# Performance work log

Hardware: AMD Instinct MI355X
Metric: run time of the kernel (lower is better)

Reference implementation:

```python
import jax, jax.numpy as jnp
import numpy as np

N = 50000      # nodes
E = 1600000    # edges (avg degree 32)
F_IN = 3       # PROTEINS num_node_features
H = 64         # dim_h
G = 512        # num graphs in batch
C = 2          # PROTEINS num_classes
BN_EPS = 1e-5


def setup_inputs() -> dict:
    key = jax.random.key(0)
    ks = iter(jax.random.split(key, 64))

    def rn(shape, s=0.1):
        return (jax.random.normal(next(ks), shape) * s).astype(jnp.float32)

    inp = {"x": rn((N, F_IN), 1.0)}
    for li, din in ((1, F_IN), (2, H), (3, H)):
        p = f"conv{li}_"
        inp[p + "w1"] = rn((din, H))
        inp[p + "b1"] = rn((H,))
        inp[p + "bn_g"] = jnp.ones((H,), jnp.float32)
        inp[p + "bn_b"] = jnp.zeros((H,), jnp.float32)
        inp[p + "bn_m"] = rn((H,))
        inp[p + "bn_v"] = jax.random.uniform(next(ks), (H,), jnp.float32, 0.5, 1.5)
        inp[p + "w2"] = rn((H, H))
        inp[p + "b2"] = rn((H,))
    inp["lin1_w"] = rn((3 * H, 3 * H))
    inp["lin1_b"] = rn((3 * H,))
    inp["lin2_w"] = rn((3 * H, C))
    inp["lin2_b"] = rn((C,))
    inp["edge_index"] = jax.random.randint(next(ks), (2, E), 0, N, jnp.int64)
    inp["batch"] = jnp.sort(jax.random.randint(next(ks), (N,), 0, G, jnp.int64))
    return inp


def gin_conv(x, src, dst, w1, b1, g, bb, m, v, w2, b2):
    # GINConv, eps=0: mlp(x + sum_{j->i} x_j); aggregate messages at target (dst)
    agg = jax.ops.segment_sum(x[src], dst, num_segments=N)  # [N, d]
    h = x + agg
    h = h @ w1 + b1
    h = (h - m) * jax.lax.rsqrt(v + BN_EPS) * g + bb  # BatchNorm1d (eval)
    h = jax.nn.relu(h)
    h = jax.nn.relu(h @ w2 + b2)
    return h


def reference(x,
              conv1_w1, conv1_b1, conv1_bn_g, conv1_bn_b, conv1_bn_m, conv1_bn_v, conv1_w2, conv1_b2,
              conv2_w1, conv2_b1, conv2_bn_g, conv2_bn_b, conv2_bn_m, conv2_bn_v, conv2_w2, conv2_b2,
              conv3_w1, conv3_b1, conv3_bn_g, conv3_bn_b, conv3_bn_m, conv3_bn_v, conv3_w2, conv3_b2,
              lin1_w, lin1_b, lin2_w, lin2_b,
              edge_index, batch):
    src, dst = edge_index[0], edge_index[1]
    h1 = gin_conv(x,  src, dst, conv1_w1, conv1_b1, conv1_bn_g, conv1_bn_b, conv1_bn_m, conv1_bn_v, conv1_w2, conv1_b2)
    h2 = gin_conv(h1, src, dst, conv2_w1, conv2_b1, conv2_bn_g, conv2_bn_b, conv2_bn_m, conv2_bn_v, conv2_w2, conv2_b2)
    h3 = gin_conv(h2, src, dst, conv3_w1, conv3_b1, conv3_bn_g, conv3_bn_b, conv3_bn_m, conv3_bn_v, conv3_w2, conv3_b2)
    # global_add_pool per graph
    p1 = jax.ops.segment_sum(h1, batch, num_segments=G)
    p2 = jax.ops.segment_sum(h2, batch, num_segments=G)
    p3 = jax.ops.segment_sum(h3, batch, num_segments=G)
    h = jnp.concatenate((p1, p2, p3), axis=1)          # [G, 3H]
    h = jax.nn.relu(h @ lin1_w + lin1_b)
    # dropout p=0.5 is identity in eval mode
    h = h @ lin2_w + lin2_b                            # [G, C]
    return (h, jax.nn.log_softmax(h, axis=1))
```

## Files before the change

### kernel.cpp

```cpp
#include <hip/hip_runtime.h>
#include <hip/hip_bf16.h>
#include <math.h>

#define N_NODES 50000
#define N_EDGES 1600000
#define H 64
#define G_GRAPHS 512
#define C_CLS 2
#define BN_EPS 1e-5f
#define NBUCK 196
#define BUCKCAP 16384
#define E4 (N_EDGES / 4)
#define CSR_BLOCKS ((E4 + 511) / 512)
#define IOP 72

typedef __attribute__((ext_vector_type(8))) short short8;
typedef __attribute__((ext_vector_type(4))) float floatx4;

__device__ __forceinline__ float bflo(unsigned int u) { return __uint_as_float(u << 16); }
__device__ __forceinline__ float bfhi(unsigned int u) { return __uint_as_float(u & 0xffff0000u); }
__device__ __forceinline__ unsigned int bf16_rne(float f) {
    unsigned int u = __float_as_uint(f);
    u += 0x7fffu + ((u >> 16) & 1u);
    return u >> 16;
}

__global__ __launch_bounds__(256) void prep_kernel(
    const float* __restrict__ w2_0, const float* __restrict__ w1_1,
    const float* __restrict__ w2_1, const float* __restrict__ w1_2,
    const float* __restrict__ w2_2, unsigned short* __restrict__ wt,
    const float* __restrict__ x, uint2* __restrict__ xb) {
    int b = blockIdx.x, t = threadIdx.x;
    if (b < 5) {
        const float* w = (b == 0) ? w2_0 : (b == 1) ? w1_1 : (b == 2) ? w2_1
                         : (b == 3) ? w1_2 : w2_2;
        unsigned short* o = wt + b * (H * H);
        for (int idx = t; idx < H * H; idx += 256) {
            int k = idx >> 6, j = idx & 63;
            o[j * H + k] = (unsigned short)bf16_rne(w[idx]);
        }
    } else {
        int node = (b - 5) * 256 + t;
        if (node < N_NODES) {
            uint2 p;
            p.x = bf16_rne(x[node * 3 + 0]) | (bf16_rne(x[node * 3 + 1]) << 16);
            p.y = bf16_rne(x[node * 3 + 2]);
            xb[node] = p;
        }
    }
}

__global__ __launch_bounds__(256) void scatter1_kernel(const int* __restrict__ src,
                                                       const int* __restrict__ dst,
                                                       int* __restrict__ gcnt,
                                                       int* __restrict__ gpacked) {
    __shared__ int bh[NBUCK];
    int t = threadIdx.x;
    if (t < NBUCK) bh[t] = 0;
    __syncthreads();
    int base = blockIdx.x * 512;

    int pkA[4], bkA[4], lrA[4]; bool vA = false;
    int pkB[4], bkB[4], lrB[4]; bool vB = false;
    {
        int i = base + t;
        if (i < E4) {
            vA = true;
            int4 s4 = ((const int4*)src)[i];
            int4 d4 = ((const int4*)dst)[i];
            bkA[0] = d4.x >> 8; pkA[0] = ((d4.x & 255) << 16) | s4.x; lrA[0] = atomicAdd(&bh[bkA[0]], 1);
            bkA[1] = d4.y >> 8; pkA[1] = ((d4.y & 255) << 16) | s4.y; lrA[1] = atomicAdd(&bh[bkA[1]], 1);
            bkA[2] = d4.z >> 8; pkA[2] = ((d4.z & 255) << 16) | s4.z; lrA[2] = atomicAdd(&bh[bkA[2]], 1);
            bkA[3] = d4.w >> 8; pkA[3] = ((d4.w & 255) << 16) | s4.w; lrA[3] = atomicAdd(&bh[bkA[3]], 1);
        }
    }
    {
        int i = base + 256 + t;
        if (i < E4) {
            vB = true;
            int4 s4 = ((const int4*)src)[i];
            int4 d4 = ((const int4*)dst)[i];
            bkB[0] = d4.x >> 8; pkB[0] = ((d4.x & 255) << 16) | s4.x; lrB[0] = atomicAdd(&bh[bkB[0]], 1);
            bkB[1] = d4.y >> 8; pkB[1] = ((d4.y & 255) << 16) | s4.y; lrB[1] = atomicAdd(&bh[bkB[1]], 1);
            bkB[2] = d4.z >> 8; pkB[2] = ((d4.z & 255) << 16) | s4.z; lrB[2] = atomicAdd(&bh[bkB[2]], 1);
            bkB[3] = d4.w >> 8; pkB[3] = ((d4.w & 255) << 16) | s4.w; lrB[3] = atomicAdd(&bh[bkB[3]], 1);
        }
    }
    __syncthreads();
    if (t < NBUCK) {
        int c = bh[t];
        bh[t] = c ? atomicAdd(&gcnt[t], c) : 0;
    }
    __syncthreads();
    if (vA) {
#pragma unroll
        for (int q = 0; q < 4; q++) gpacked[bkA[q] * BUCKCAP + bh[bkA[q]] + lrA[q]] = pkA[q];
    }
    if (vB) {
#pragma unroll
        for (int q = 0; q < 4; q++) gpacked[bkB[q] * BUCKCAP + bh[bkB[q]] + lrB[q]] = pkB[q];
    }
}

__global__ __launch_bounds__(256) void bcsr_kernel(const int* __restrict__ gpacked,
                                                   const int* __restrict__ gcnt,
                                                   int* __restrict__ row_start,
                                                   int* __restrict__ edge_src) {
    __shared__ int cnt[256];
    __shared__ int pref[256];
    int b = blockIdx.x;
    int t = threadIdx.x;

    int v = (t < NBUCK) ? gcnt[t] : 0;
    pref[t] = v;
    __syncthreads();
    for (int off = 1; off < 256; off <<= 1) {
        int u = 0;
        if (t >= off) u = pref[t - off];
        __syncthreads();
        if (t >= off) pref[t] += u;
        __syncthreads();
    }
    int bs = (b > 0) ? pref[b - 1] : 0;
    int cnt_b = gcnt[b];
    if (b == 0 && t == 0) row_start[N_NODES] = N_EDGES;
    __syncthreads();

    const int* gp = gpacked + (size_t)b * BUCKCAP;
    cnt[t] = 0;
    __syncthreads();
    for (int i = t; i < cnt_b; i += 256) atomicAdd(&cnt[gp[i] >> 16], 1);
    __syncthreads();
    int c = cnt[t];
    pref[t] = c;
    __syncthreads();
    for (int off = 1; off < 256; off <<= 1) {
        int u = 0;
        if (t >= off) u = pref[t - off];
        __syncthreads();
        if (t >= off) pref[t] += u;
        __syncthreads();
    }
    int excl = pref[t] - c;
    int node = b * 256 + t;
    if (node < N_NODES) row_start[node] = bs + excl;
    cnt[t] = excl;
    __syncthreads();
    for (int i = t; i < cnt_b; i += 256) {
        int p = gp[i];
        int pos = atomicAdd(&cnt[p >> 16], 1);
        edge_src[bs + pos] = p & 0xffff;
    }
}

#define RED3(A) { A += __shfl_xor(A, 8); A += __shfl_xor(A, 16); A += __shfl_xor(A, 32); }
#define RED6(A) { A += __shfl_xor(A, 1); A += __shfl_xor(A, 2); A += __shfl_xor(A, 4); \
                  A += __shfl_xor(A, 8); A += __shfl_xor(A, 16); A += __shfl_xor(A, 32); }

__global__ __launch_bounds__(512) void gin1_fused16_kernel(
    const float* __restrict__ x, const uint2* __restrict__ xb,
    const int* __restrict__ row_start, const int* __restrict__ edge_src,
    const float* __restrict__ w1, const float* __restrict__ b1,
    const float* __restrict__ bn_g, const float* __restrict__ bn_b,
    const float* __restrict__ bn_m, const float* __restrict__ bn_v,
    const unsigned short* __restrict__ w2t, const float* __restrict__ b2,
    __hip_bfloat16* __restrict__ hout, const int* __restrict__ batch,
    float* __restrict__ pool) {
    __shared__ unsigned short s_mid[16 * IOP];
    __shared__ int s_bat[16];

    int tid = threadIdx.x;
    int wave = tid >> 6, j = tid & 63;
    int nodebase = blockIdx.x * 16;
    if (tid < 16) s_bat[tid] = batch[nodebase + tid];

    float wj0 = w1[j], wj1 = w1[H + j], wj2 = w1[2 * H + j];
    float sc = rsqrtf(bn_v[j] + BN_EPS) * bn_g[j];
    float sh = bn_b[j] - bn_m[j] * sc;
    float bj = b1[j];

    int n0 = nodebase + wave * 2;
    int rs0 = row_start[n0];
    int re0 = row_start[n0 + 1];
    int re1 = row_start[n0 + 2];
    int c0 = re0 - rs0;
    int total = re1 - rs0;

    float a00 = 0.f, a01 = 0.f, a02 = 0.f;
    float a10 = 0.f, a11 = 0.f, a12 = 0.f;
    for (int base = 0; base < total; base += 64) {
        int idx = rs0 + base + j;
        if (idx < re1) {
            uint2 p = xb[edge_src[idx]];
            if (base + j < c0) { a00 += bflo(p.x); a01 += bfhi(p.x); a02 += bflo(p.y); }
            else               { a10 += bflo(p.x); a11 += bfhi(p.x); a12 += bflo(p.y); }
        }
    }
    RED6(a00) RED6(a01) RED6(a02)
    RED6(a10) RED6(a11) RED6(a12)
    {
        float in0 = a00 + x[n0 * 3 + 0];
        float in1 = a01 + x[n0 * 3 + 1];
        float in2 = a02 + x[n0 * 3 + 2];
        float m = bj + in0 * wj0 + in1 * wj1 + in2 * wj2;
        m = fmaxf(m * sc + sh, 0.f);
        s_mid[(wave * 2) * IOP + j] = (unsigned short)bf16_rne(m);
    }
    {
        int n1 = n0 + 1;
        float in0 = a10 + x[n1 * 3 + 0];
        float in1 = a11 + x[n1 * 3 + 1];
        float in2 = a12 + x[n1 * 3 + 2];
        float m = bj + in0 * wj0 + in1 * wj1 + in2 * wj2;
        m = fmaxf(m * sc + sh, 0.f);
        s_mid[(wave * 2 + 1) * IOP + j] = (unsigned short)bf16_rne(m);
    }
    __syncthreads();

    if (wave == 0) {
        int quad = j >> 4, l15 = j & 15;
        float bb2[4];
#pragma unroll
        for (int jt = 0; jt < 4; jt++) bb2[jt] = b2[jt * 16 + l15];

        short8 m0 = *(const short8*)&s_mid[l15 * IOP + quad * 8];
        short8 m1 = *(const short8*)&s_mid[l15 * IOP + quad * 8 + 32];
        int bq0 = s_bat[quad * 4], bq3 = s_bat[quad * 4 + 3];
#pragma unroll
        for (int jt = 0; jt < 4; jt++) {
            short8 b0 = *(const short8*)&w2t[(jt * 16 + l15) * H + quad * 8];
            short8 bv = *(const short8*)&w2t[(jt * 16 + l15) * H + quad * 8 + 32];
            floatx4 c = {0.f, 0.f, 0.f, 0.f};
            c = __builtin_amdgcn_mfma_f32_16x16x32_bf16(m0, b0, c, 0, 0, 0);
            c = __builtin_amdgcn_mfma_f32_16x16x32_bf16(m1, bv, c, 0, 0, 0);
            float vv[4];
#pragma unroll
            for (int r = 0; r < 4; r++) {
                float v = fmaxf(c[r] + bb2[jt], 0.f);
                vv[r] = v;
                s_mid[(quad * 4 + r) * IOP + jt * 16 + l15] = (unsigned short)bf16_rne(v);
            }
            int jj = jt * 16 + l15;
            if (bq0 == bq3) {
                atomicAdd(&pool[bq0 * 192 + jj], (vv[0] + vv[1]) + (vv[2] + vv[3]));
            } else {
                atomicAdd(&pool[s_bat[quad * 4 + 0] * 192 + jj], vv[0]);
                atomicAdd(&pool[s_bat[quad * 4 + 1] * 192 + jj], vv[1]);
                atomicAdd(&pool[s_bat[quad * 4 + 2] * 192 + jj], vv[2]);
                atomicAdd(&pool[s_bat[quad * 4 + 3] * 192 + jj], vv[3]);
            }
        }
        unsigned short* ho = (unsigned short*)hout;
#pragma unroll
        for (int cc = 0; cc < 2; cc++) {
            int r = cc * 8 + (j >> 3);
            short8 v = *(const short8*)&s_mid[r * IOP + (j & 7) * 8];
            *(short8*)(ho + (size_t)(nodebase + r) * H + (j & 7) * 8) = v;
        }
    }
}

#define ACC8(R, A0, A1, A2, A3, A4, A5, A6, A7) { \
    A0 += bflo(R.x); A1 += bfhi(R.x); A2 += bflo(R.y); A3 += bfhi(R.y); \
    A4 += bflo(R.z); A5 += bfhi(R.z); A6 += bflo(R.w); A7 += bfhi(R.w); }

#define GROUP_ACC(R, r) { \
    if ((r) < lim) { \
        if ((base + (r)) < c0) { ACC8(R, a00, a01, a02, a03, a04, a05, a06, a07) } \
        else                   { ACC8(R, a10, a11, a12, a13, a14, a15, a16, a17) } \
    } }

__global__ __launch_bounds__(512) void gin_fused16_kernel(
    const __hip_bfloat16* __restrict__ hin, const int* __restrict__ row_start,
    const int* __restrict__ edge_src,
    const unsigned short* __restrict__ w1t, const float* __restrict__ b1,
    const float* __restrict__ bn_g, const float* __restrict__ bn_b,
    const float* __restrict__ bn_m, const float* __restrict__ bn_v,
    const unsigned short* __restrict__ w2t, const float* __restrict__ b2,
    __hip_bfloat16* __restrict__ hout, const int* __restrict__ batch,
    float* __restrict__ pool) {
    __shared__ unsigned short s_xs[16 * IOP];
    __shared__ unsigned short s_mid[16 * IOP];
    __shared__ int s_bat[16];

    int tid = threadIdx.x;
    int wave = tid >> 6, j = tid & 63;
    int o = j >> 3, jo = j & 7;
    int nodebase = blockIdx.x * 16;
    if (tid < 16) s_bat[tid] = batch[nodebase + tid];

    const char* hb = (const char*)hin;

    int n0 = nodebase + wave * 2;
    int rs0 = row_start[n0];
    int re0 = row_start[n0 + 1];
    int re1 = row_start[n0 + 2];
    int c0 = re0 - rs0;
    int total = re1 - rs0;

    float a00 = 0.f, a01 = 0.f, a02 = 0.f, a03 = 0.f, a04 = 0.f, a05 = 0.f, a06 = 0.f, a07 = 0.f;
    float a10 = 0.f, a11 = 0.f, a12 = 0.f, a13 = 0.f, a14 = 0.f, a15 = 0.f, a16 = 0.f, a17 = 0.f;

    for (int base = 0; base < total; base += 64) {
        int idx = rs0 + base + j;
        int sv = (idx < re1) ? edge_src[idx] : 0;
        int lim = min(64, total - base);
#pragma unroll
        for (int i = 0; i < 64; i += 32) {
            if (i >= lim) break;
            int r0 = i + o, r1 = i + 8 + o, r2 = i + 16 + o, r3 = i + 24 + o;
            int s0 = __shfl(sv, r0);
            int s1 = __shfl(sv, r1);
            int s2 = __shfl(sv, r2);
            int s3 = __shfl(sv, r3);
            uint4 R0 = *(const uint4*)(hb + (size_t)s0 * 128 + jo * 16);
            uint4 R1 = *(const uint4*)(hb + (size_t)s1 * 128 + jo * 16);
            uint4 R2 = *(const uint4*)(hb + (size_t)s2 * 128 + jo * 16);
            uint4 R3 = *(const uint4*)(hb + (size_t)s3 * 128 + jo * 16);
            GROUP_ACC(R0, r0)
            GROUP_ACC(R1, r1)
            GROUP_ACC(R2, r2)
            GROUP_ACC(R3, r3)
        }
    }
    RED3(a00) RED3(a01) RED3(a02) RED3(a03) RED3(a04) RED3(a05) RED3(a06) RED3(a07)
    RED3(a10) RED3(a11) RED3(a12) RED3(a13) RED3(a14) RED3(a15) RED3(a16) RED3(a17)

    if (o < 2) {
        int nl = wave * 2 + o;
        float r0 = (o == 0) ? a00 : a10, r1 = (o == 0) ? a01 : a11;
        float r2 = (o == 0) ? a02 : a12, r3 = (o == 0) ? a03 : a13;
        float r4 = (o == 0) ? a04 : a14, r5 = (o == 0) ? a05 : a15;
        float r6 = (o == 0) ? a06 : a16, r7 = (o == 0) ? a07 : a17;
        uint4 raw = *(const uint4*)(hb + (size_t)(nodebase + nl) * 128 + jo * 16);
        r0 += bflo(raw.x); r1 += bfhi(raw.x);
        r2 += bflo(raw.y); r3 += bfhi(raw.y);
        r4 += bflo(raw.z); r5 += bfhi(raw.z);
        r6 += bflo(raw.w); r7 += bfhi(raw.w);
        uint4 ov;
        ov.x = bf16_rne(r0) | (bf16_rne(r1) << 16);
        ov.y = bf16_rne(r2) | (bf16_rne(r3) << 16);
        ov.z = bf16_rne(r4) | (bf16_rne(r5) << 16);
        ov.w = bf16_rne(r6) | (bf16_rne(r7) << 16);
        *(uint4*)&s_xs[nl * IOP + jo * 8] = ov;
    }
    __syncthreads();

    if (wave == 0) {
        int quad = j >> 4, l15 = j & 15;
        float scl[4], sht[4], bb1[4], bb2[4];
#pragma unroll
        for (int jt = 0; jt < 4; jt++) {
            int jj = jt * 16 + l15;
            float sc = rsqrtf(bn_v[jj] + BN_EPS) * bn_g[jj];
            scl[jt] = sc;
            sht[jt] = bn_b[jj] - bn_m[jj] * sc;
            bb1[jt] = b1[jj];
            bb2[jt] = b2[jj];
        }
        short8 a0 = *(const short8*)&s_xs[l15 * IOP + quad * 8];
        short8 a1 = *(const short8*)&s_xs[l15 * IOP + quad * 8 + 32];
#pragma unroll
        for (int jt = 0; jt < 4; jt++) {
            short8 b0 = *(const short8*)&w1t[(jt * 16 + l15) * H + quad * 8];
            short8 bv = *(const short8*)&w1t[(jt * 16 + l15) * H + quad * 8 + 32];
            floatx4 c = {0.f, 0.f, 0.f, 0.f};
            c = __builtin_amdgcn_mfma_f32_16x16x32_bf16(a0, b0, c, 0, 0, 0);
            c = __builtin_amdgcn_mfma_f32_16x16x32_bf16(a1, bv, c, 0, 0, 0);
#pragma unroll
            for (int r = 0; r < 4; r++) {
                float v = (c[r] + bb1[jt]) * scl[jt] + sht[jt];
                v = fmaxf(v, 0.f);
                s_mid[(quad * 4 + r) * IOP + jt * 16 + l15] = (unsigned short)bf16_rne(v);
            }
        }
        short8 m0 = *(const short8*)&s_mid[l15 * IOP + quad * 8];
        short8 m1 = *(const short8*)&s_mid[l15 * IOP + quad * 8 + 32];
        int bq0 = s_bat[quad * 4], bq3 = s_bat[quad * 4 + 3];
#pragma unroll
        for (int jt = 0; jt < 4; jt++) {
            short8 b0 = *(const short8*)&w2t[(jt * 16 + l15) * H + quad * 8];
            short8 bv = *(const short8*)&w2t[(jt * 16 + l15) * H + quad * 8 + 32];
            floatx4 c = {0.f, 0.f, 0.f, 0.f};
            c = __builtin_amdgcn_mfma_f32_16x16x32_bf16(m0, b0, c, 0, 0, 0);
            c = __builtin_amdgcn_mfma_f32_16x16x32_bf16(m1, bv, c, 0, 0, 0);
            float vv[4];
#pragma unroll
            for (int r = 0; r < 4; r++) {
                float v = fmaxf(c[r] + bb2[jt], 0.f);
                vv[r] = v;
                s_xs[(quad * 4 + r) * IOP + jt * 16 + l15] = (unsigned short)bf16_rne(v);
            }
            int jj = jt * 16 + l15;
            if (bq0 == bq3) {
                atomicAdd(&pool[bq0 * 192 + jj], (vv[0] + vv[1]) + (vv[2] + vv[3]));
            } else {
                atomicAdd(&pool[s_bat[quad * 4 + 0] * 192 + jj], vv[0]);
                atomicAdd(&pool[s_bat[quad * 4 + 1] * 192 + jj], vv[1]);
                atomicAdd(&pool[s_bat[quad * 4 + 2] * 192 + jj], vv[2]);
                atomicAdd(&pool[s_bat[quad * 4 + 3] * 192 + jj], vv[3]);
            }
        }
        unsigned short* ho = (unsigned short*)hout;
#pragma unroll
        for (int cc = 0; cc < 2; cc++) {
            int r = cc * 8 + (j >> 3);
            short8 v = *(const short8*)&s_xs[r * IOP + (j & 7) * 8];
            *(short8*)(ho + (size_t)(nodebase + r) * H + (j & 7) * 8) = v;
        }
    }
}

__global__ __launch_bounds__(192) void head_kernel(
    const float* __restrict__ pool,
    const float* __restrict__ lin1_w, const float* __restrict__ lin1_b,
    const float* __restrict__ lin2_w, const float* __restrict__ lin2_b,
    float* __restrict__ out) {
    __shared__ float s_row[3 * H];
    __shared__ float s_mid[3 * H];
    __shared__ float s_z[C_CLS];

    int g = blockIdx.x;
    int j = threadIdx.x;
    s_row[j] = pool[g * 192 + j];
    __syncthreads();

    float acc = lin1_b[j];
    for (int k = 0; k < 3 * H; k++) acc += s_row[k] * lin1_w[k * (3 * H) + j];
    s_mid[j] = fmaxf(acc, 0.f);
    __syncthreads();

    if (j < C_CLS) {
        float z = lin2_b[j];
        for (int k = 0; k < 3 * H; k++) z += s_mid[k] * lin2_w[k * C_CLS + j];
        s_z[j] = z;
    }
    __syncthreads();
    if (j < C_CLS) {
        float z0 = s_z[0], z1 = s_z[1];
        float mx = fmaxf(z0, z1);
        float lse = mx + logf(expf(z0 - mx) + expf(z1 - mx));
        out[g * C_CLS + j] = s_z[j];
        out[G_GRAPHS * C_CLS + g * C_CLS + j] = s_z[j] - lse;
    }
}

extern "C" void kernel_launch(void* const* d_in, const int* in_sizes, int n_in,
                              void* d_out, int out_size, void* d_ws, size_t ws_size,
                              hipStream_t stream) {
    const float* x = (const float*)d_in[0];
    const float* cw1[3], *cb1[3], *cg[3], *cbb[3], *cm[3], *cv[3], *cw2[3], *cb2[3];
    for (int l = 0; l < 3; l++) {
        int b = 1 + 8 * l;
        cw1[l] = (const float*)d_in[b + 0];
        cb1[l] = (const float*)d_in[b + 1];
        cg[l]  = (const float*)d_in[b + 2];
        cbb[l] = (const float*)d_in[b + 3];
        cm[l]  = (const float*)d_in[b + 4];
        cv[l]  = (const float*)d_in[b + 5];
        cw2[l] = (const float*)d_in[b + 6];
        cb2[l] = (const float*)d_in[b + 7];
    }
    const float* lin1_w = (const float*)d_in[25];
    const float* lin1_b = (const float*)d_in[26];
    const float* lin2_w = (const float*)d_in[27];
    const float* lin2_b = (const float*)d_in[28];
    const int* edge_index = (const int*)d_in[29];
    const int* batch = (const int*)d_in[30];
    const int* src = edge_index;
    const int* dst = edge_index + N_EDGES;
    float* out = (float*)d_out;

    int* edge_src = (int*)d_ws;
    int* gpacked = edge_src + N_EDGES;
    int* gcnt = gpacked + (size_t)NBUCK * BUCKCAP;
    float* pool = (float*)(gcnt + NBUCK);
    int* row_start = (int*)(pool + G_GRAPHS * 3 * H);
    uintptr_t hp = (uintptr_t)(row_start + N_NODES + 2);
    hp = (hp + 127) & ~(uintptr_t)127;
    unsigned short* wt = (unsigned short*)hp;
    uint2* xb = (uint2*)(wt + 5 * H * H);
    __hip_bfloat16* h1 = (__hip_bfloat16*)(xb + N_NODES);
    __hip_bfloat16* h2 = h1 + (size_t)N_NODES * H;
    __hip_bfloat16* h3 = h2 + (size_t)N_NODES * H;

    const unsigned short* w2t_0 = wt + 0 * H * H;
    const unsigned short* w1t_1 = wt + 1 * H * H;
    const unsigned short* w2t_1 = wt + 2 * H * H;
    const unsigned short* w1t_2 = wt + 3 * H * H;
    const unsigned short* w2t_2 = wt + 4 * H * H;

    hipMemsetAsync(gcnt, 0, NBUCK * sizeof(int) + G_GRAPHS * 3 * H * sizeof(float), stream);
    prep_kernel<<<5 + (N_NODES + 255) / 256, 256, 0, stream>>>(
        cw2[0], cw1[1], cw2[1], cw1[2], cw2[2], wt, x, xb);
    scatter1_kernel<<<CSR_BLOCKS, 256, 0, stream>>>(src, dst, gcnt, gpacked);
    bcsr_kernel<<<NBUCK, 256, 0, stream>>>(gpacked, gcnt, row_start, edge_src);

    const int fgrid = N_NODES / 16;

    gin1_fused16_kernel<<<fgrid, 512, 0, stream>>>(x, xb, row_start, edge_src,
        cw1[0], cb1[0], cg[0], cbb[0], cm[0], cv[0], w2t_0, cb2[0], h1, batch, pool);
    gin_fused16_kernel<<<fgrid, 512, 0, stream>>>(h1, row_start, edge_src,
        w1t_1, cb1[1], cg[1], cbb[1], cm[1], cv[1], w2t_1, cb2[1], h2, batch, pool + 64);
    gin_fused16_kernel<<<fgrid, 512, 0, stream>>>(h2, row_start, edge_src,
        w1t_2, cb1[2], cg[2], cbb[2], cm[2], cv[2], w2t_2, cb2[2], h3, batch, pool + 128);
    head_kernel<<<G_GRAPHS, 3 * H, 0, stream>>>(pool,
        lin1_w, lin1_b, lin2_w, lin2_b, out);
}
```

Measured before the change: 289.4 us.

## Merge prep and scatter kernels, split MFMA across waves, decouple per-node gathers

The weight/x prep kernel and the edge bucket-scatter kernel become one launch, which also zeroes a padding row in h1/h2. The layer-1 gather now loops per node, and in the hidden layers each wave gathers its two nodes independently, with out-of-range lanes pointed at the zero row instead of branching per edge. The MLP matmuls are spread across four waves (one 16-column tile each) rather than done by a single wave, and launch bounds of 4 blocks per CU are added. The aim is less launch overhead, more parallel MFMA work in the epilogue and less divergence in the gather, at the cost of extra block barriers and a __syncthreads that only waves 0-3 reach inside the wave<4 branch (waves 4-7 call one in the else branch).

```diff
diff --git a/kernel.cpp b/kernel.cpp
--- a/kernel.cpp
+++ b/kernel.cpp
@@ -11,8 +11,11 @@
 #define NBUCK 196
 #define BUCKCAP 16384
 #define E4 (N_EDGES / 4)
-#define CSR_BLOCKS ((E4 + 511) / 512)
+#define SCHUNKS ((E4 + 511) / 512)
+#define XCHUNKS ((N_NODES + 255) / 256)
 #define IOP 72
+#define ZROW N_NODES
+#define HSTRIDE ((N_NODES + 1) * H)
 
 typedef __attribute__((ext_vector_type(8))) short short8;
 typedef __attribute__((ext_vector_type(4))) float floatx4;
@@ -25,80 +28,85 @@
     return u >> 16;
 }
 
-__global__ __launch_bounds__(256) void prep_kernel(
+#define RED3(A) { A += __shfl_xor(A, 8); A += __shfl_xor(A, 16); A += __shfl_xor(A, 32); }
+#define RED6(A) { A += __shfl_xor(A, 1); A += __shfl_xor(A, 2); A += __shfl_xor(A, 4); \
+                  A += __shfl_xor(A, 8); A += __shfl_xor(A, 16); A += __shfl_xor(A, 32); }
+
+__global__ __launch_bounds__(256) void prepscatter_kernel(
+    const int* __restrict__ src, const int* __restrict__ dst,
+    int* __restrict__ gcnt, int* __restrict__ gpacked,
     const float* __restrict__ w2_0, const float* __restrict__ w1_1,
     const float* __restrict__ w2_1, const float* __restrict__ w1_2,
     const float* __restrict__ w2_2, unsigned short* __restrict__ wt,
-    const float* __restrict__ x, uint2* __restrict__ xb) {
+    const float* __restrict__ x, uint2* __restrict__ xb,
+    __hip_bfloat16* __restrict__ h1, __hip_bfloat16* __restrict__ h2) {
     int b = blockIdx.x, t = threadIdx.x;
-    if (b < 5) {
-        const float* w = (b == 0) ? w2_0 : (b == 1) ? w1_1 : (b == 2) ? w2_1
-                         : (b == 3) ? w1_2 : w2_2;
-        unsigned short* o = wt + b * (H * H);
+    if (b < SCHUNKS) {
+        __shared__ int bh[NBUCK];
+        if (t < NBUCK) bh[t] = 0;
+        __syncthreads();
+        int base = b * 512;
+        int pkA[4], bkA[4], lrA[4]; bool vA = false;
+        int pkB[4], bkB[4], lrB[4]; bool vB = false;
+        {
+            int i = base + t;
+            if (i < E4) {
+                vA = true;
+                int4 s4 = ((const int4*)src)[i];
+                int4 d4 = ((const int4*)dst)[i];
+                bkA[0] = d4.x >> 8; pkA[0] = ((d4.x & 255) << 16) | s4.x; lrA[0] = atomicAdd(&bh[bkA[0]], 1);
+                bkA[1] = d4.y >> 8; pkA[1] = ((d4.y & 255) << 16) | s4.y; lrA[1] = atomicAdd(&bh[bkA[1]], 1);
+                bkA[2] = d4.z >> 8; pkA[2] = ((d4.z & 255) << 16) | s4.z; lrA[2] = atomicAdd(&bh[bkA[2]], 1);
+                bkA[3] = d4.w >> 8; pkA[3] = ((d4.w & 255) << 16) | s4.w; lrA[3] = atomicAdd(&bh[bkA[3]], 1);
+            }
+        }
+        {
+            int i = base + 256 + t;
+            if (i < E4) {
+                vB = true;
+                int4 s4 = ((const int4*)src)[i];
+                int4 d4 = ((const int4*)dst)[i];
+                bkB[0] = d4.x >> 8; pkB[0] = ((d4.x & 255) << 16) | s4.x; lrB[0] = atomicAdd(&bh[bkB[0]], 1);
+                bkB[1] = d4.y >> 8; pkB[1] = ((d4.y & 255) << 16) | s4.y; lrB[1] = atomicAdd(&bh[bkB[1]], 1);
+                bkB[2] = d4.z >> 8; pkB[2] = ((d4.z & 255) << 16) | s4.z; lrB[2] = atomicAdd(&bh[bkB[2]], 1);
+                bkB[3] = d4.w >> 8; pkB[3] = ((d4.w & 255) << 16) | s4.w; lrB[3] = atomicAdd(&bh[bkB[3]], 1);
+            }
+        }
+        __syncthreads();
+        if (t < NBUCK) {
+            int c = bh[t];
+            bh[t] = c ? atomicAdd(&gcnt[t], c) : 0;
+        }
+        __syncthreads();
+        if (vA) {
+#pragma unroll
+            for (int q = 0; q < 4; q++) gpacked[bkA[q] * BUCKCAP + bh[bkA[q]] + lrA[q]] = pkA[q];
+        }
+        if (vB) {
+#pragma unroll
+            for (int q = 0; q < 4; q++) gpacked[bkB[q] * BUCKCAP + bh[bkB[q]] + lrB[q]] = pkB[q];
+        }
+    } else if (b < SCHUNKS + 5) {
+        int w_id = b - SCHUNKS;
+        const float* w = (w_id == 0) ? w2_0 : (w_id == 1) ? w1_1 : (w_id == 2) ? w2_1
+                         : (w_id == 3) ? w1_2 : w2_2;
+        unsigned short* o = wt + w_id * (H * H);
         for (int idx = t; idx < H * H; idx += 256) {
-            int k = idx >> 6, j = idx & 63;
-            o[j * H + k] = (unsigned short)bf16_rne(w[idx]);
-        }
-    } else {
-        int node = (b - 5) * 256 + t;
+            int k = idx >> 6, jc = idx & 63;
+            o[jc * H + k] = (unsigned short)bf16_rne(w[idx]);
+        }
+    } else if (b < SCHUNKS + 5 + XCHUNKS) {
+        int node = (b - SCHUNKS - 5) * 256 + t;
         if (node < N_NODES) {
             uint2 p;
             p.x = bf16_rne(x[node * 3 + 0]) | (bf16_rne(x[node * 3 + 1]) << 16);
             p.y = bf16_rne(x[node * 3 + 2]);
             xb[node] = p;
         }
-    }
-}
-
-__global__ __launch_bounds__(256) void scatter1_kernel(const int* __restrict__ src,
-                                                       const int* __restrict__ dst,
-                                                       int* __restrict__ gcnt,
-                                                       int* __restrict__ gpacked) {
-    __shared__ int bh[NBUCK];
-    int t = threadIdx.x;
-    if (t < NBUCK) bh[t] = 0;
-    __syncthreads();
-    int base = blockIdx.x * 512;
-
-    int pkA[4], bkA[4], lrA[4]; bool vA = false;
-    int pkB[4], bkB[4], lrB[4]; bool vB = false;
-    {
-        int i = base + t;
-        if (i < E4) {
-            vA = true;
-            int4 s4 = ((const int4*)src)[i];
-            int4 d4 = ((const int4*)dst)[i];
-            bkA[0] = d4.x >> 8; pkA[0] = ((d4.x & 255) << 16) | s4.x; lrA[0] = atomicAdd(&bh[bkA[0]], 1);
-            bkA[1] = d4.y >> 8; pkA[1] = ((d4.y & 255) << 16) | s4.y; lrA[1] = atomicAdd(&bh[bkA[1]], 1);
-            bkA[2] = d4.z >> 8; pkA[2] = ((d4.z & 255) << 16) | s4.z; lrA[2] = atomicAdd(&bh[bkA[2]], 1);
-            bkA[3] = d4.w >> 8; pkA[3] = ((d4.w & 255) << 16) | s4.w; lrA[3] = atomicAdd(&bh[bkA[3]], 1);
-        }
-    }
-    {
-        int i = base + 256 + t;
-        if (i < E4) {
-            vB = true;
-            int4 s4 = ((const int4*)src)[i];
-            int4 d4 = ((const int4*)dst)[i];
-            bkB[0] = d4.x >> 8; pkB[0] = ((d4.x & 255) << 16) | s4.x; lrB[0] = atomicAdd(&bh[bkB[0]], 1);
-            bkB[1] = d4.y >> 8; pkB[1] = ((d4.y & 255) << 16) | s4.y; lrB[1] = atomicAdd(&bh[bkB[1]], 1);
-            bkB[2] = d4.z >> 8; pkB[2] = ((d4.z & 255) << 16) | s4.z; lrB[2] = atomicAdd(&bh[bkB[2]], 1);
-            bkB[3] = d4.w >> 8; pkB[3] = ((d4.w & 255) << 16) | s4.w; lrB[3] = atomicAdd(&bh[bkB[3]], 1);
-        }
-    }
-    __syncthreads();
-    if (t < NBUCK) {
-        int c = bh[t];
-        bh[t] = c ? atomicAdd(&gcnt[t], c) : 0;
-    }
-    __syncthreads();
-    if (vA) {
-#pragma unroll
-        for (int q = 0; q < 4; q++) gpacked[bkA[q] * BUCKCAP + bh[bkA[q]] + lrA[q]] = pkA[q];
-    }
-    if (vB) {
-#pragma unroll
-        for (int q = 0; q < 4; q++) gpacked[bkB[q] * BUCKCAP + bh[bkB[q]] + lrB[q]] = pkB[q];
+    } else {
+        uint4 z = {0u, 0u, 0u, 0u};
+        if (t < 8) ((uint4*)((unsigned short*)h1 + (size_t)ZROW * H))[t] = z;
+        else if (t < 16) ((uint4*)((unsigned short*)h2 + (size_t)ZROW * H))[t - 8] = z;
     }
 }
 
@@ -152,10 +160,6 @@
         edge_src[bs + pos] = p & 0xffff;
     }
 }
-
-#define RED3(A) { A += __shfl_xor(A, 8); A += __shfl_xor(A, 16); A += __shfl_xor(A, 32); }
-#define RED6(A) { A += __shfl_xor(A, 1); A += __shfl_xor(A, 2); A += __shfl_xor(A, 4); \
-                  A += __shfl_xor(A, 8); A += __shfl_xor(A, 16); A += __shfl_xor(A, 32); }
 
 __global__ __launch_bounds__(512) void gin1_fused16_kernel(
     const float* __restrict__ x, const uint2* __restrict__ xb,
@@ -167,10 +171,12 @@
     __hip_bfloat16* __restrict__ hout, const int* __restrict__ batch,
     float* __restrict__ pool) {
     __shared__ unsigned short s_mid[16 * IOP];
+    __shared__ unsigned short s_xs[16 * IOP];
     __shared__ int s_bat[16];
 
     int tid = threadIdx.x;
     int wave = tid >> 6, j = tid & 63;
+    int quad = j >> 4, l15 = j & 15;
     int nodebase = blockIdx.x * 16;
     if (tid < 16) s_bat[tid] = batch[nodebase + tid];
 
@@ -179,98 +185,67 @@
     float sh = bn_b[j] - bn_m[j] * sc;
     float bj = b1[j];
 
-    int n0 = nodebase + wave * 2;
-    int rs0 = row_start[n0];
-    int re0 = row_start[n0 + 1];
-    int re1 = row_start[n0 + 2];
-    int c0 = re0 - rs0;
-    int total = re1 - rs0;
-
-    float a00 = 0.f, a01 = 0.f, a02 = 0.f;
-    float a10 = 0.f, a11 = 0.f, a12 = 0.f;
-    for (int base = 0; base < total; base += 64) {
-        int idx = rs0 + base + j;
-        if (idx < re1) {
-            uint2 p = xb[edge_src[idx]];
-            if (base + j < c0) { a00 += bflo(p.x); a01 += bfhi(p.x); a02 += bflo(p.y); }
-            else               { a10 += bflo(p.x); a11 += bfhi(p.x); a12 += bflo(p.y); }
-        }
-    }
-    RED6(a00) RED6(a01) RED6(a02)
-    RED6(a10) RED6(a11) RED6(a12)
-    {
-        float in0 = a00 + x[n0 * 3 + 0];
-        float in1 = a01 + x[n0 * 3 + 1];
-        float in2 = a02 + x[n0 * 3 + 2];
+    for (int nl = wave * 2; nl < wave * 2 + 2; nl++) {
+        int node = nodebase + nl;
+        int rs = row_start[node], re = row_start[node + 1];
+        float a0 = 0.f, a1 = 0.f, a2 = 0.f;
+        for (int t2 = rs + j; t2 < re; t2 += 64) {
+            uint2 p = xb[edge_src[t2]];
+            a0 += bflo(p.x); a1 += bfhi(p.x); a2 += bflo(p.y);
+        }
+        RED6(a0) RED6(a1) RED6(a2)
+        float in0 = a0 + x[node * 3 + 0];
+        float in1 = a1 + x[node * 3 + 1];
+        float in2 = a2 + x[node * 3 + 2];
         float m = bj + in0 * wj0 + in1 * wj1 + in2 * wj2;
         m = fmaxf(m * sc + sh, 0.f);
-        s_mid[(wave * 2) * IOP + j] = (unsigned short)bf16_rne(m);
-    }
-    {
-        int n1 = n0 + 1;
-        float in0 = a10 + x[n1 * 3 + 0];
-        float in1 = a11 + x[n1 * 3 + 1];
-        float in2 = a12 + x[n1 * 3 + 2];
-        float m = bj + in0 * wj0 + in1 * wj1 + in2 * wj2;
-        m = fmaxf(m * sc + sh, 0.f);
-        s_mid[(wave * 2 + 1) * IOP + j] = (unsigned short)bf16_rne(m);
-    }
-    __syncthreads();
-
-    if (wave == 0) {
-        int quad = j >> 4, l15 = j & 15;
-        float bb2[4];
-#pragma unroll
-        for (int jt = 0; jt < 4; jt++) bb2[jt] = b2[jt * 16 + l15];
-
+        s_mid[nl * IOP + j] = (unsigned short)bf16_rne(m);
+    }
+    __syncthreads();
+
+    if (wave < 4) {
+        int jj = wave * 16 + l15;
+        float bb2 = b2[jj];
         short8 m0 = *(const short8*)&s_mid[l15 * IOP + quad * 8];
         short8 m1 = *(const short8*)&s_mid[l15 * IOP + quad * 8 + 32];
+        short8 b0 = *(const short8*)&w2t[jj * H + quad * 8];
+        short8 bv = *(const short8*)&w2t[jj * H + quad * 8 + 32];
+        floatx4 c = {0.f, 0.f, 0.f, 0.f};
+        c = __builtin_amdgcn_mfma_f32_16x16x32_bf16(m0, b0, c, 0, 0, 0);
+        c = __builtin_amdgcn_mfma_f32_16x16x32_bf16(m1, bv, c, 0, 0, 0);
+        float vv[4];
+#pragma unroll
+        for (int r = 0; r < 4; r++) {
+            vv[r] = fmaxf(c[r] + bb2, 0.f);
+            s_xs[(quad * 4 + r) * IOP + jj] = (unsigned short)bf16_rne(vv[r]);
+        }
         int bq0 = s_bat[quad * 4], bq3 = s_bat[quad * 4 + 3];
-#pragma unroll
-        for (int jt = 0; jt < 4; jt++) {
-            short8 b0 = *(const short8*)&w2t[(jt * 16 + l15) * H + quad * 8];
-            short8 bv = *(const short8*)&w2t[(jt * 16 + l15) * H + quad * 8 + 32];
-            floatx4 c = {0.f, 0.f, 0.f, 0.f};
-            c = __builtin_amdgcn_mfma_f32_16x16x32_bf16(m0, b0, c, 0, 0, 0);
-            c = __builtin_amdgcn_mfma_f32_16x16x32_bf16(m1, bv, c, 0, 0, 0);
-            float vv[4];
-#pragma unroll
-            for (int r = 0; r < 4; r++) {
-                float v = fmaxf(c[r] + bb2[jt], 0.f);
-                vv[r] = v;
-                s_mid[(quad * 4 + r) * IOP + jt * 16 + l15] = (unsigned short)bf16_rne(v);
-            }
-            int jj = jt * 16 + l15;
-            if (bq0 == bq3) {
-                atomicAdd(&pool[bq0 * 192 + jj], (vv[0] + vv[1]) + (vv[2] + vv[3]));
-            } else {
-                atomicAdd(&pool[s_bat[quad * 4 + 0] * 192 + jj], vv[0]);
-                atomicAdd(&pool[s_bat[quad * 4 + 1] * 192 + jj], vv[1]);
-                atomicAdd(&pool[s_bat[quad * 4 + 2] * 192 + jj], vv[2]);
-                atomicAdd(&pool[s_bat[quad * 4 + 3] * 192 + jj], vv[3]);
-            }
-        }
-        unsigned short* ho = (unsigned short*)hout;
-#pragma unroll
-        for (int cc = 0; cc < 2; cc++) {
-            int r = cc * 8 + (j >> 3);
-            short8 v = *(const short8*)&s_mid[r * IOP + (j & 7) * 8];
-            *(short8*)(ho + (size_t)(nodebase + r) * H + (j & 7) * 8) = v;
-        }
-    }
-}
-
-#define ACC8(R, A0, A1, A2, A3, A4, A5, A6, A7) { \
-    A0 += bflo(R.x); A1 += bfhi(R.x); A2 += bflo(R.y); A3 += bfhi(R.y); \
-    A4 += bflo(R.z); A5 += bfhi(R.z); A6 += bflo(R.w); A7 += bfhi(R.w); }
-
-#define GROUP_ACC(R, r) { \
-    if ((r) < lim) { \
-        if ((base + (r)) < c0) { ACC8(R, a00, a01, a02, a03, a04, a05, a06, a07) } \
-        else                   { ACC8(R, a10, a11, a12, a13, a14, a15, a16, a17) } \
-    } }
-
-__global__ __launch_bounds__(512) void gin_fused16_kernel(
+        if (bq0 == bq3) {
+            atomicAdd(&pool[bq0 * 192 + jj], (vv[0] + vv[1]) + (vv[2] + vv[3]));
+        } else {
+            atomicAdd(&pool[s_bat[quad * 4 + 0] * 192 + jj], vv[0]);
+            atomicAdd(&pool[s_bat[quad * 4 + 1] * 192 + jj], vv[1]);
+            atomicAdd(&pool[s_bat[quad * 4 + 2] * 192 + jj], vv[2]);
+            atomicAdd(&pool[s_bat[quad * 4 + 3] * 192 + jj], vv[3]);
+        }
+    }
+    __syncthreads();
+
+    if (wave < 2) {
+        int r = wave * 8 + (j >> 3);
+        short8 v = *(const short8*)&s_xs[r * IOP + (j & 7) * 8];
+        *(short8*)((unsigned short*)hout + (size_t)(nodebase + r) * H + (j & 7) * 8) = v;
+    }
+}
+
+#define ACCA(R) { \
+    a0 += bflo(R.x); a1 += bfhi(R.x); a2 += bflo(R.y); a3 += bfhi(R.y); \
+    a4 += bflo(R.z); a5 += bfhi(R.z); a6 += bflo(R.w); a7 += bfhi(R.w); }
+#define ACCB(R) { \
+    b0 += bflo(R.x); b1 += bfhi(R.x); b2 += bflo(R.y); b3 += bfhi(R.y); \
+    b4 += bflo(R.z); b5 += bfhi(R.z); b6 += bflo(R.w); b7 += bfhi(R.w); }
+
+__global__ __launch_bounds__(512, 4) void gin_fused16_kernel(
     const __hip_bfloat16* __restrict__ hin, const int* __restrict__ row_start,
     const int* __restrict__ edge_src,
     const unsigned short* __restrict__ w1t, const float* __restrict__ b1,
@@ -286,52 +261,66 @@
     int tid = threadIdx.x;
     int wave = tid >> 6, j = tid & 63;
     int o = j >> 3, jo = j & 7;
+    int quad = j >> 4, l15 = j & 15;
     int nodebase = blockIdx.x * 16;
     if (tid < 16) s_bat[tid] = batch[nodebase + tid];
 
     const char* hb = (const char*)hin;
 
     int n0 = nodebase + wave * 2;
-    int rs0 = row_start[n0];
-    int re0 = row_start[n0 + 1];
-    int re1 = row_start[n0 + 2];
-    int c0 = re0 - rs0;
-    int total = re1 - rs0;
-
-    float a00 = 0.f, a01 = 0.f, a02 = 0.f, a03 = 0.f, a04 = 0.f, a05 = 0.f, a06 = 0.f, a07 = 0.f;
-    float a10 = 0.f, a11 = 0.f, a12 = 0.f, a13 = 0.f, a14 = 0.f, a15 = 0.f, a16 = 0.f, a17 = 0.f;
-
-    for (int base = 0; base < total; base += 64) {
-        int idx = rs0 + base + j;
-        int sv = (idx < re1) ? edge_src[idx] : 0;
-        int lim = min(64, total - base);
-#pragma unroll
-        for (int i = 0; i < 64; i += 32) {
-            if (i >= lim) break;
-            int r0 = i + o, r1 = i + 8 + o, r2 = i + 16 + o, r3 = i + 24 + o;
-            int s0 = __shfl(sv, r0);
-            int s1 = __shfl(sv, r1);
-            int s2 = __shfl(sv, r2);
-            int s3 = __shfl(sv, r3);
-            uint4 R0 = *(const uint4*)(hb + (size_t)s0 * 128 + jo * 16);
-            uint4 R1 = *(const uint4*)(hb + (size_t)s1 * 128 + jo * 16);
-            uint4 R2 = *(const uint4*)(hb + (size_t)s2 * 128 + jo * 16);
-            uint4 R3 = *(const uint4*)(hb + (size_t)s3 * 128 + jo * 16);
-            GROUP_ACC(R0, r0)
-            GROUP_ACC(R1, r1)
-            GROUP_ACC(R2, r2)
-            GROUP_ACC(R3, r3)
-        }
-    }
-    RED3(a00) RED3(a01) RED3(a02) RED3(a03) RED3(a04) RED3(a05) RED3(a06) RED3(a07)
-    RED3(a10) RED3(a11) RED3(a12) RED3(a13) RED3(a14) RED3(a15) RED3(a16) RED3(a17)
+    int rsA = row_start[n0];
+    int rsB = row_start[n0 + 1];
+    int reB = row_start[n0 + 2];
+    int cntA = rsB - rsA, cntB = reB - rsB;
+    int cmax = max(cntA, cntB);
+
+    float a0 = 0.f, a1 = 0.f, a2 = 0.f, a3 = 0.f, a4 = 0.f, a5 = 0.f, a6 = 0.f, a7 = 0.f;
+    float b0 = 0.f, b1v = 0.f, b2v = 0.f, b3 = 0.f, b4 = 0.f, b5 = 0.f, b6 = 0.f, b7 = 0.f;
+#define b1 b1v
+#define b2 b2v
+    for (int base = 0; base < cmax; base += 64) {
+        int svA = (base + j < cntA) ? edge_src[rsA + base + j] : ZROW;
+        int svB = (base + j < cntB) ? edge_src[rsB + base + j] : ZROW;
+#pragma unroll
+        for (int g = 0; g < 64; g += 32) {
+            bool doA = (base + g) < cntA;
+            bool doB = (base + g) < cntB;
+            uint4 RA0, RA1, RA2, RA3, RB0, RB1, RB2, RB3;
+            if (doA) {
+                int s0 = __shfl(svA, g + o);
+                int s1 = __shfl(svA, g + 8 + o);
+                int s2 = __shfl(svA, g + 16 + o);
+                int s3 = __shfl(svA, g + 24 + o);
+                RA0 = *(const uint4*)(hb + (size_t)s0 * 128 + jo * 16);
+                RA1 = *(const uint4*)(hb + (size_t)s1 * 128 + jo * 16);
+                RA2 = *(const uint4*)(hb + (size_t)s2 * 128 + jo * 16);
+                RA3 = *(const uint4*)(hb + (size_t)s3 * 128 + jo * 16);
+            }
+            if (doB) {
+                int s0 = __shfl(svB, g + o);
+                int s1 = __shfl(svB, g + 8 + o);
+                int s2 = __shfl(svB, g + 16 + o);
+                int s3 = __shfl(svB, g + 24 + o);
+                RB0 = *(const uint4*)(hb + (size_t)s0 * 128 + jo * 16);
+                RB1 = *(const uint4*)(hb + (size_t)s1 * 128 + jo * 16);
+                RB2 = *(const uint4*)(hb + (size_t)s2 * 128 + jo * 16);
+                RB3 = *(const uint4*)(hb + (size_t)s3 * 128 + jo * 16);
+            }
+            if (doA) { ACCA(RA0) ACCA(RA1) ACCA(RA2) ACCA(RA3) }
+            if (doB) { ACCB(RB0) ACCB(RB1) ACCB(RB2) ACCB(RB3) }
+        }
+    }
+#undef b1
+#undef b2
+    RED3(a0) RED3(b0) RED3(a1) RED3(b1v) RED3(a2) RED3(b2v) RED3(a3) RED3(b3)
+    RED3(a4) RED3(b4) RED3(a5) RED3(b5) RED3(a6) RED3(b6) RED3(a7) RED3(b7)
 
     if (o < 2) {
         int nl = wave * 2 + o;
-        float r0 = (o == 0) ? a00 : a10, r1 = (o == 0) ? a01 : a11;
-        float r2 = (o == 0) ? a02 : a12, r3 = (o == 0) ? a03 : a13;
-        float r4 = (o == 0) ? a04 : a14, r5 = (o == 0) ? a05 : a15;
-        float r6 = (o == 0) ? a06 : a16, r7 = (o == 0) ? a07 : a17;
+        float r0 = (o == 0) ? a0 : b0, r1 = (o == 0) ? a1 : b1v;
+        float r2 = (o == 0) ? a2 : b2v, r3 = (o == 0) ? a3 : b3;
+        float r4 = (o == 0) ? a4 : b4, r5 = (o == 0) ? a5 : b5;
+        float r6 = (o == 0) ? a6 : b6, r7 = (o == 0) ? a7 : b7;
         uint4 raw = *(const uint4*)(hb + (size_t)(nodebase + nl) * 128 + jo * 16);
         r0 += bflo(raw.x); r1 += bfhi(raw.x);
         r2 += bflo(raw.y); r3 += bfhi(raw.y);
@@ -346,68 +335,56 @@
     }
     __syncthreads();
 
-    if (wave == 0) {
-        int quad = j >> 4, l15 = j & 15;
-        float scl[4], sht[4], bb1[4], bb2[4];
-#pragma unroll
-        for (int jt = 0; jt < 4; jt++) {
-            int jj = jt * 16 + l15;
-            float sc = rsqrtf(bn_v[jj] + BN_EPS) * bn_g[jj];
-            scl[jt] = sc;
-            sht[jt] = bn_b[jj] - bn_m[jj] * sc;
-            bb1[jt] = b1[jj];
-            bb2[jt] = b2[jj];
-        }
-        short8 a0 = *(const short8*)&s_xs[l15 * IOP + quad * 8];
-        short8 a1 = *(const short8*)&s_xs[l15 * IOP + quad * 8 + 32];
-#pragma unroll
-        for (int jt = 0; jt < 4; jt++) {
-            short8 b0 = *(const short8*)&w1t[(jt * 16 + l15) * H + quad * 8];
-            short8 bv = *(const short8*)&w1t[(jt * 16 + l15) * H + quad * 8 + 32];
-            floatx4 c = {0.f, 0.f, 0.f, 0.f};
-            c = __builtin_amdgcn_mfma_f32_16x16x32_bf16(a0, b0, c, 0, 0, 0);
-            c = __builtin_amdgcn_mfma_f32_16x16x32_bf16(a1, bv, c, 0, 0, 0);
-#pragma unroll
-            for (int r = 0; r < 4; r++) {
-                float v = (c[r] + bb1[jt]) * scl[jt] + sht[jt];
-                v = fmaxf(v, 0.f);
-                s_mid[(quad * 4 + r) * IOP + jt * 16 + l15] = (unsigned short)bf16_rne(v);
-            }
-        }
-        short8 m0 = *(const short8*)&s_mid[l15 * IOP + quad * 8];
-        short8 m1 = *(const short8*)&s_mid[l15 * IOP + quad * 8 + 32];
+    if (wave < 4) {
+        int jj = wave * 16 + l15;
+        float scv = rsqrtf(bn_v[jj] + BN_EPS) * bn_g[jj];
+        float shv = bn_b[jj] - bn_m[jj] * scv;
+        float bb1 = b1[jj], bb2 = b2[jj];
+        short8 A0 = *(const short8*)&s_xs[l15 * IOP + quad * 8];
+        short8 A1 = *(const short8*)&s_xs[l15 * IOP + quad * 8 + 32];
+        short8 w10 = *(const short8*)&w1t[jj * H + quad * 8];
+        short8 w11 = *(const short8*)&w1t[jj * H + quad * 8 + 32];
+        floatx4 c = {0.f, 0.f, 0.f, 0.f};
+        c = __builtin_amdgcn_mfma_f32_16x16x32_bf16(A0, w10, c, 0, 0, 0);
+        c = __builtin_amdgcn_mfma_f32_16x16x32_bf16(A1, w11, c, 0, 0, 0);
+#pragma unroll
+        for (int r = 0; r < 4; r++) {
+            float v = (c[r] + bb1) * scv + shv;
+            v = fmaxf(v, 0.f);
+            s_mid[(quad * 4 + r) * IOP + jj] = (unsigned short)bf16_rne(v);
+        }
+        __syncthreads();
+        short8 M0 = *(const short8*)&s_mid[l15 * IOP + quad * 8];
+        short8 M1 = *(const short8*)&s_mid[l15 * IOP + quad * 8 + 32];
+        short8 w20 = *(const short8*)&w2t[jj * H + quad * 8];
+        short8 w21 = *(const short8*)&w2t[jj * H + quad * 8 + 32];
+        floatx4 c2 = {0.f, 0.f, 0.f, 0.f};
+        c2 = __builtin_amdgcn_mfma_f32_16x16x32_bf16(M0, w20, c2, 0, 0, 0);
+        c2 = __builtin_amdgcn_mfma_f32_16x16x32_bf16(M1, w21, c2, 0, 0, 0);
+        float vv[4];
+#pragma unroll
+        for (int r = 0; r < 4; r++) {
+            vv[r] = fmaxf(c2[r] + bb2, 0.f);
+            s_xs[(quad * 4 + r) * IOP + jj] = (unsigned short)bf16_rne(vv[r]);
+        }
         int bq0 = s_bat[quad * 4], bq3 = s_bat[quad * 4 + 3];
-#pragma unroll
-        for (int jt = 0; jt < 4; jt++) {
-            short8 b0 = *(const short8*)&w2t[(jt * 16 + l15) * H + quad * 8];
-            short8 bv = *(const short8*)&w2t[(jt * 16 + l15) * H + quad * 8 + 32];
-            floatx4 c = {0.f, 0.f, 0.f, 0.f};
-            c = __builtin_amdgcn_mfma_f32_16x16x32_bf16(m0, b0, c, 0, 0, 0);
-            c = __builtin_amdgcn_mfma_f32_16x16x32_bf16(m1, bv, c, 0, 0, 0);
-            float vv[4];
-#pragma unroll
-            for (int r = 0; r < 4; r++) {
-                float v = fmaxf(c[r] + bb2[jt], 0.f);
-                vv[r] = v;
-                s_xs[(quad * 4 + r) * IOP + jt * 16 + l15] = (unsigned short)bf16_rne(v);
-            }
-            int jj = jt * 16 + l15;
-            if (bq0 == bq3) {
-                atomicAdd(&pool[bq0 * 192 + jj], (vv[0] + vv[1]) + (vv[2] + vv[3]));
-            } else {
-                atomicAdd(&pool[s_bat[quad * 4 + 0] * 192 + jj], vv[0]);
-                atomicAdd(&pool[s_bat[quad * 4 + 1] * 192 + jj], vv[1]);
-                atomicAdd(&pool[s_bat[quad * 4 + 2] * 192 + jj], vv[2]);
-                atomicAdd(&pool[s_bat[quad * 4 + 3] * 192 + jj], vv[3]);
-            }
-        }
-        unsigned short* ho = (unsigned short*)hout;
-#pragma unroll
-        for (int cc = 0; cc < 2; cc++) {
-            int r = cc * 8 + (j >> 3);
-            short8 v = *(const short8*)&s_xs[r * IOP + (j & 7) * 8];
-            *(short8*)(ho + (size_t)(nodebase + r) * H + (j & 7) * 8) = v;
-        }
+        if (bq0 == bq3) {
+            atomicAdd(&pool[bq0 * 192 + jj], (vv[0] + vv[1]) + (vv[2] + vv[3]));
+        } else {
+            atomicAdd(&pool[s_bat[quad * 4 + 0] * 192 + jj], vv[0]);
+            atomicAdd(&pool[s_bat[quad * 4 + 1] * 192 + jj], vv[1]);
+            atomicAdd(&pool[s_bat[quad * 4 + 2] * 192 + jj], vv[2]);
+            atomicAdd(&pool[s_bat[quad * 4 + 3] * 192 + jj], vv[3]);
+        }
+    } else {
+        __syncthreads();
+    }
+    __syncthreads();
+
+    if (wave < 2) {
+        int r = wave * 8 + (j >> 3);
+        short8 v = *(const short8*)&s_xs[r * IOP + (j & 7) * 8];
+        *(short8*)((unsigned short*)hout + (size_t)(nodebase + r) * H + (j & 7) * 8) = v;
     }
 }
 
@@ -481,8 +458,8 @@
     unsigned short* wt = (unsigned short*)hp;
     uint2* xb = (uint2*)(wt + 5 * H * H);
     __hip_bfloat16* h1 = (__hip_bfloat16*)(xb + N_NODES);
-    __hip_bfloat16* h2 = h1 + (size_t)N_NODES * H;
-    __hip_bfloat16* h3 = h2 + (size_t)N_NODES * H;
+    __hip_bfloat16* h2 = h1 + (size_t)HSTRIDE;
+    __hip_bfloat16* h3 = h2 + (size_t)HSTRIDE;
 
     const unsigned short* w2t_0 = wt + 0 * H * H;
     const unsigned short* w1t_1 = wt + 1 * H * H;
@@ -490,10 +467,10 @@
     const unsigned short* w1t_2 = wt + 3 * H * H;
     const unsigned short* w2t_2 = wt + 4 * H * H;
 
-    hipMemsetAsync(gcnt, 0, NBUCK * sizeof(int) + G_GRAPHS * 3 * H * sizeof(float), stream);
-    prep_kernel<<<5 + (N_NODES + 255) / 256, 256, 0, stream>>>(
-        cw2[0], cw1[1], cw2[1], cw1[2], cw2[2], wt, x, xb);
-    scatter1_kernel<<<CSR_BLOCKS, 256, 0, stream>>>(src, dst, gcnt, gpacked);
+    hipMemsetAsync(gcnt, 0, NBUCK * sizeof(int) + (size_t)G_GRAPHS * 3 * H * sizeof(float),
+                   stream);
+    prepscatter_kernel<<<SCHUNKS + 5 + XCHUNKS + 1, 256, 0, stream>>>(
+        src, dst, gcnt, gpacked, cw2[0], cw1[1], cw2[1], cw1[2], cw2[2], wt, x, xb, h1, h2);
     bcsr_kernel<<<NBUCK, 256, 0, stream>>>(gpacked, gcnt, row_start, edge_src);
 
     const int fgrid = N_NODES / 16;
```

New measurement: 314.3 us. 1.09x slower.
